# Optimization experiments

Measured on AMD Instinct MI355X. Metric: run time of the kernel, lower is better.

The kernel has to match this reference:

```python
import jax, jax.numpy as jnp
import numpy as np

N_NODES = 100000
N_EDGES = 200000
HIDDEN = 384


def setup_inputs() -> dict:
    key = jax.random.key(0)
    ks = jax.random.split(key, 8)
    x = jax.random.normal(ks[0], (N_NODES, HIDDEN), dtype=jnp.float32)
    # row (source) covers every node at least once so degree >= 1 everywhere
    row_extra = jax.random.randint(ks[1], (N_EDGES - N_NODES,), 0, N_NODES)
    row = jnp.concatenate([jnp.arange(N_NODES), row_extra]).astype(jnp.int64)
    col = jax.random.randint(ks[2], (N_EDGES,), 0, N_NODES).astype(jnp.int64)
    edge_index = jnp.stack([row, col])  # [2, E]
    s = 1.0 / np.sqrt(HIDDEN)
    W1 = jax.random.normal(ks[3], (HIDDEN, HIDDEN), dtype=jnp.float32) * s
    b1 = jax.random.normal(ks[4], (HIDDEN,), dtype=jnp.float32) * s
    W2 = jax.random.normal(ks[5], (HIDDEN, HIDDEN), dtype=jnp.float32) * s
    b2 = jax.random.normal(ks[6], (HIDDEN,), dtype=jnp.float32) * s
    return {"x": x, "edge_index": edge_index, "W1": W1, "b1": b1, "W2": W2, "b2": b2}


def _gcn_layer(x, row, col, W, b):
    n = x.shape[0]
    x = x @ W.T + b  # Linear (torch convention: y = x W^T + b)
    # degree over row (source) only, as in the original message()
    deg = jax.ops.segment_sum(jnp.ones_like(row, dtype=x.dtype), row, num_segments=n)
    dis = deg ** -0.5  # deg>=1 by construction
    norm = dis[row] * dis[col]  # [E]
    msgs = norm[:, None] * x[row]  # gather + scale
    return jax.ops.segment_sum(msgs, col, num_segments=n)  # scatter-add into targets


def reference(x, edge_index, W1, b1, W2, b2):
    row, col = edge_index[0], edge_index[1]
    x = _gcn_layer(x, row, col, W1, b1)
    x = _gcn_layer(x, row, col, W2, b2)
    return x
```

## Files before the change

### kernel.cpp

```cpp
#include <hip/hip_runtime.h>
#include <hip/hip_bf16.h>
#include <cstdint>

#define N_HID 384
#define BM 128
#define BN 128
#define BK 64
#define KTILES 6

typedef __attribute__((ext_vector_type(8))) short bf16x8;
typedef __attribute__((ext_vector_type(4))) float f32x4;

static __device__ __forceinline__ short f2bf(float f) {
    union { __hip_bfloat16 h; short s; } u;
    u.h = __float2bfloat16(f);
    return u.s;
}

static __device__ __forceinline__ void gload_lds16(const void* g, void* l) {
    __builtin_amdgcn_global_load_lds(
        (const __attribute__((address_space(1))) void*)g,
        (__attribute__((address_space(3))) void*)l,
        16, 0, 0);
}

__global__ __launch_bounds__(256) void k_hist(const int* __restrict__ row,
                                              const int* __restrict__ col,
                                              int* __restrict__ deg,
                                              int* __restrict__ cnt, int E) {
    int i = blockIdx.x * 256 + threadIdx.x;
    if (i < E) {
        atomicAdd(&deg[row[i]], 1);
        atomicAdd(&cnt[col[i]], 1);
    }
}

__global__ __launch_bounds__(256) void k_dis(const int* __restrict__ deg,
                                             float* __restrict__ dis, int N) {
    int i = blockIdx.x * 256 + threadIdx.x;
    if (i < N) dis[i] = rsqrtf((float)deg[i]);
}

__global__ __launch_bounds__(256) void k_cvt(const float* __restrict__ in,
                                             short* __restrict__ out, int n4) {
    int i = blockIdx.x * 256 + threadIdx.x;
    if (i < n4) {
        float4 v = reinterpret_cast<const float4*>(in)[i];
        short4 s = make_short4(f2bf(v.x), f2bf(v.y), f2bf(v.z), f2bf(v.w));
        reinterpret_cast<short4*>(out)[i] = s;
    }
}


__global__ __launch_bounds__(256) void k_scan1(const int* __restrict__ cnt,
                                               int* __restrict__ offs,
                                               int* __restrict__ bsum, int N) {
    __shared__ int s[256];
    const int t = threadIdx.x;
    const int base = blockIdx.x * 1024 + t * 4;
    int v[4], tot = 0;
    #pragma unroll
    for (int i = 0; i < 4; i++) { v[i] = (base + i < N) ? cnt[base + i] : 0; tot += v[i]; }
    s[t] = tot;
    __syncthreads();
    #pragma unroll
    for (int off = 1; off < 256; off <<= 1) {
        int x = (t >= off) ? s[t - off] : 0;
        __syncthreads();
        s[t] += x;
        __syncthreads();
    }
    if (t == 255) bsum[blockIdx.x] = s[255];
    int run = s[t] - tot;
    #pragma unroll
    for (int i = 0; i < 4; i++) { if (base + i < N) offs[base + i] = run; run += v[i]; }
}

__global__ __launch_bounds__(256) void k_scan2(int* __restrict__ bsum, int nb) {
    __shared__ int s[256];
    const int t = threadIdx.x;
    int v = (t < nb) ? bsum[t] : 0;
    s[t] = v;
    __syncthreads();
    #pragma unroll
    for (int off = 1; off < 256; off <<= 1) {
        int x = (t >= off) ? s[t - off] : 0;
        __syncthreads();
        s[t] += x;
        __syncthreads();
    }
    if (t < nb) bsum[t] = s[t] - v;
}

__global__ __launch_bounds__(256) void k_scan3(int* __restrict__ offs,
                                               const int* __restrict__ bsum, int N) {
    int i = blockIdx.x * 256 + threadIdx.x;
    if (i < N) offs[i] += bsum[i >> 10];
}

__global__ __launch_bounds__(256) void k_fill(const int* __restrict__ row,
                                              const int* __restrict__ col,
                                              const float* __restrict__ dis,
                                              const int* __restrict__ offs,
                                              int* __restrict__ cur,
                                              int2* __restrict__ srcnrm, int E) {
    int e = blockIdx.x * 256 + threadIdx.x;
    if (e >= E) return;
    int r = row[e], c = col[e];
    int slot = offs[c] + atomicAdd(&cur[c], 1);
    int2 p;
    p.x = r;
    p.y = __float_as_int(dis[r] * dis[c]);
    srcnrm[slot] = p;
}

__global__ __launch_bounds__(256) void k_gemm(const short* __restrict__ A,
                                              const short* __restrict__ W,
                                              const float* __restrict__ bias,
                                              short* __restrict__ out, int M, int MT) {
    __shared__ short As[2][BM][BK];
    __shared__ short Bs[2][BN][BK];
    const int t = threadIdx.x;
    const int bid = blockIdx.x;
    const int m_idx = ((bid >> 3) / 3) * 8 + (bid & 7);
    const int n_idx = (bid >> 3) % 3;
    if (m_idx >= MT) return;
    const int m0 = m_idx * BM, n0 = n_idx * BN;
    const int wave = t >> 6, lane = t & 63;
    const int wm = (wave & 1) * 64, wn = (wave >> 1) * 64;
    const int l16 = lane & 15, quad = lane >> 4;
    const int srow = lane >> 3;
    const int sg8 = ((lane & 7) ^ srow) * 8;
    const int sbase = wave * 8;

    f32x4 acc[4][4] = {};

    auto stage = [&](int b, int kt) {
        #pragma unroll
        for (int p = 0; p < 4; p++) {
            int gm = m0 + p * 32 + sbase + srow;
            gm = gm < M ? gm : M - 1;
            gload_lds16(A + (size_t)gm * N_HID + kt + sg8, &As[b][p * 32 + sbase][0]);
        }
        #pragma unroll
        for (int p = 0; p < 4; p++) {
            int gn = n0 + p * 32 + sbase + srow;
            gload_lds16(W + (size_t)gn * N_HID + kt + sg8, &Bs[b][p * 32 + sbase][0]);
        }
    };

    stage(0, 0);
    #pragma unroll
    for (int kt6 = 0; kt6 < KTILES; kt6++) {
        const int b = kt6 & 1;
        __syncthreads();
        if (kt6 + 1 < KTILES) stage(1 - b, (kt6 + 1) * BK);
        #pragma unroll
        for (int kk = 0; kk < 2; kk++) {
            const int gc = kk * 4 + quad;
            bf16x8 af[4], bfr[4];
            #pragma unroll
            for (int i = 0; i < 4; i++) {
                int rr = wm + i * 16 + l16;
                af[i] = *reinterpret_cast<const bf16x8*>(&As[b][rr][(gc ^ (l16 & 7)) * 8]);
            }
            #pragma unroll
            for (int j = 0; j < 4; j++) {
                int rr = wn + j * 16 + l16;
                bfr[j] = *reinterpret_cast<const bf16x8*>(&Bs[b][rr][(gc ^ (l16 & 7)) * 8]);
            }
            #pragma unroll
            for (int i = 0; i < 4; i++)
                #pragma unroll
                for (int j = 0; j < 4; j++)
                    acc[i][j] = __builtin_amdgcn_mfma_f32_16x16x32_bf16(af[i], bfr[j], acc[i][j], 0, 0, 0);
        }
    }

    __syncthreads();
    short* eps = &As[0][0][0] + wave * 4096;
    #pragma unroll
    for (int j = 0; j < 4; j++) {
        float bv = bias[n0 + wn + j * 16 + l16];
        #pragma unroll
        for (int i = 0; i < 4; i++)
            #pragma unroll
            for (int r = 0; r < 4; r++) {
                int rw = i * 16 + quad * 4 + r;
                int colw = j * 16 + l16;
                int chs = ((colw >> 3) + (rw & 7) + (rw >> 3)) & 7;
                eps[rw * 64 + chs * 8 + (colw & 7)] = f2bf(acc[i][j][r] + bv);
            }
    }
    __syncthreads();
    const int r8 = lane >> 3, ch2 = lane & 7;
    #pragma unroll
    for (int pass = 0; pass < 8; pass++) {
        int rw = pass * 8 + r8;
        int chs = (ch2 + r8 + pass) & 7;
        bf16x8 v = *reinterpret_cast<const bf16x8*>(&eps[rw * 64 + chs * 8]);
        int gm = m0 + wm + rw;
        if (gm < M)
            *reinterpret_cast<bf16x8*>(out + (size_t)gm * N_HID + n0 + wn + ch2 * 8) = v;
    }
}

template <bool BF16OUT>
__global__ __launch_bounds__(256) void k_gather(const short* __restrict__ h,
                                                const int2* __restrict__ srcnrm,
                                                const int* __restrict__ offs,
                                                const int* __restrict__ cur,
                                                void* __restrict__ outv, int N) {
    int node = (blockIdx.x * 256 + threadIdx.x) >> 6;
    if (node >= N) return;
    int lane = threadIdx.x & 63;
    int start = offs[node];
    int ecnt  = cur[node];
    float2 acc[3] = {};
    for (int i = 0; i < ecnt; i++) {
        int2 p = srcnrm[start + i];
        int s = p.x;
        float w = __int_as_float(p.y);
        const unsigned int* hr = reinterpret_cast<const unsigned int*>(h + (size_t)s * N_HID);
        #pragma unroll
        for (int k = 0; k < 3; k++) {
            unsigned int pk = hr[lane + 64 * k];
            acc[k].x += w * __uint_as_float(pk << 16);
            acc[k].y += w * __uint_as_float(pk & 0xffff0000u);
        }
    }
    if (BF16OUT) {
        unsigned int* oc = reinterpret_cast<unsigned int*>(outv) + (size_t)node * 192;
        #pragma unroll
        for (int k = 0; k < 3; k++) {
            unsigned int lo = (unsigned int)(unsigned short)f2bf(acc[k].x);
            unsigned int hi = (unsigned int)(unsigned short)f2bf(acc[k].y);
            oc[lane + 64 * k] = lo | (hi << 16);
        }
    } else {
        float2* oc = reinterpret_cast<float2*>(outv) + (size_t)node * 192;
        #pragma unroll
        for (int k = 0; k < 3; k++) oc[lane + 64 * k] = acc[k];
    }
}

extern "C" void kernel_launch(void* const* d_in, const int* in_sizes, int n_in,
                              void* d_out, int out_size, void* d_ws, size_t ws_size,
                              hipStream_t stream) {
    const float* x  = (const float*)d_in[0];
    const int*   ei = (const int*)d_in[1];
    const float* W1 = (const float*)d_in[2];
    const float* b1 = (const float*)d_in[3];
    const float* W2 = (const float*)d_in[4];
    const float* b2 = (const float*)d_in[5];
    float* out = (float*)d_out;

    const int N = in_sizes[0] / N_HID;
    const int E = in_sizes[1] / 2;
    const int* row = ei;
    const int* col = ei + E;
    const int nb = (N + 1023) / 1024;

    short* xb = (short*)d_out;
    short* a1 = (short*)d_out + (size_t)N * N_HID;

    auto al = [](size_t v) { return (v + 255) & ~(size_t)255; };
    char* ws = (char*)d_ws;
    size_t o = 0;
    int*   deg    = (int*)(ws + o);   o += al((size_t)N * 4);
    int*   offs   = (int*)(ws + o);   o += al((size_t)N * 4);
    float* dis    = (float*)(ws + o); o += al((size_t)N * 4);
    int*   bsum   = (int*)(ws + o);   o += al((size_t)nb * 4);
    int2*  srcnrm = (int2*)(ws + o);  o += al((size_t)E * 8);
    short* w1b    = (short*)(ws + o); o += al((size_t)N_HID * N_HID * 2);
    short* w2b    = (short*)(ws + o); o += al((size_t)N_HID * N_HID * 2);
    short* h      = (short*)(ws + o);
    int*   cur    = deg;

    hipMemsetAsync(deg, 0, al((size_t)N * 4) + (size_t)N * 4, stream);
    k_hist<<<(E + 255) / 256, 256, 0, stream>>>(row, col, deg, offs, E);
    k_dis<<<(N + 255) / 256, 256, 0, stream>>>(deg, dis, N);

    k_scan1<<<nb, 256, 0, stream>>>(offs, offs, bsum, N);
    k_scan2<<<1, 256, 0, stream>>>(bsum, nb);
    k_scan3<<<(N + 255) / 256, 256, 0, stream>>>(offs, bsum, N);
    hipMemsetAsync(cur, 0, (size_t)N * 4, stream);
    k_fill<<<(E + 255) / 256, 256, 0, stream>>>(row, col, dis, offs, cur, srcnrm, E);

    const int x4 = (int)((size_t)N * N_HID / 4);
    const int w4 = N_HID * N_HID / 4;
    k_cvt<<<(x4 + 255) / 256, 256, 0, stream>>>(x, xb, x4);
    k_cvt<<<(w4 + 255) / 256, 256, 0, stream>>>(W1, w1b, w4);
    k_cvt<<<(w4 + 255) / 256, 256, 0, stream>>>(W2, w2b, w4);

    const int MT = (N + BM - 1) / BM;
    const int gblocks = ((MT + 7) / 8) * 24;
    const int gat_blocks = (int)(((size_t)N * 64 + 255) / 256);

    k_gemm<<<gblocks, 256, 0, stream>>>(xb, w1b, b1, h, N, MT);
    k_gather<true><<<gat_blocks, 256, 0, stream>>>(h, srcnrm, offs, cur, a1, N);

    k_gemm<<<gblocks, 256, 0, stream>>>(a1, w2b, b2, h, N, MT);
    k_gather<false><<<gat_blocks, 256, 0, stream>>>(h, srcnrm, offs, cur, out, N);
}
```

Baseline: 491.1 us.

## Reorder GCN as aggregate-then-transform with fused W2·W1 weight and bias folding

Uses linearity to run both sparse aggregations on raw x first. The first gather reads fp32 x directly, so the separate bf16 conversion of x is dropped. The two dense GEMMs are collapsed into a single GEMM against a precomputed W2·W1 product, and the bias terms are folded back in through per-node aggregated normalisation sums (dvec, ddvec) and W2·b1. This removes one large GEMM and the x conversion pass. In exchange the first gather moves fp32 rows instead of bf16, and rounding the product weight and the gathered features to bf16 changes precision.

```diff
diff --git a/kernel.cpp b/kernel.cpp
--- a/kernel.cpp
+++ b/kernel.cpp
@@ -35,22 +35,6 @@
     }
 }
 
-__global__ __launch_bounds__(256) void k_dis(const int* __restrict__ deg,
-                                             float* __restrict__ dis, int N) {
-    int i = blockIdx.x * 256 + threadIdx.x;
-    if (i < N) dis[i] = rsqrtf((float)deg[i]);
-}
-
-__global__ __launch_bounds__(256) void k_cvt(const float* __restrict__ in,
-                                             short* __restrict__ out, int n4) {
-    int i = blockIdx.x * 256 + threadIdx.x;
-    if (i < n4) {
-        float4 v = reinterpret_cast<const float4*>(in)[i];
-        short4 s = make_short4(f2bf(v.x), f2bf(v.y), f2bf(v.z), f2bf(v.w));
-        reinterpret_cast<short4*>(out)[i] = s;
-    }
-}
-
 
 __global__ __launch_bounds__(256) void k_scan1(const int* __restrict__ cnt,
                                                int* __restrict__ offs,
@@ -100,7 +84,7 @@
 
 __global__ __launch_bounds__(256) void k_fill(const int* __restrict__ row,
                                               const int* __restrict__ col,
-                                              const float* __restrict__ dis,
+                                              const int* __restrict__ deg,
                                               const int* __restrict__ offs,
                                               int* __restrict__ cur,
                                               int2* __restrict__ srcnrm, int E) {
@@ -110,14 +94,56 @@
     int slot = offs[c] + atomicAdd(&cur[c], 1);
     int2 p;
     p.x = r;
-    p.y = __float_as_int(dis[r] * dis[c]);
+    p.y = __float_as_int(rsqrtf((float)deg[r]) * rsqrtf((float)deg[c]));
     srcnrm[slot] = p;
 }
 
+__global__ __launch_bounds__(256) void k_prep(const float* __restrict__ W1,
+                                              const float* __restrict__ W2,
+                                              const float* __restrict__ b1,
+                                              short* __restrict__ w1t,
+                                              short* __restrict__ w2b,
+                                              float* __restrict__ wb1) {
+    const int bid = blockIdx.x, t = threadIdx.x;
+    if (bid < 144) {
+        __shared__ short tl[32][33];
+        const int tx = bid % 12, ty = bid / 12;
+        const int c = t & 31, r8 = t >> 5;
+        #pragma unroll
+        for (int rr = 0; rr < 32; rr += 8)
+            tl[c][rr + r8] = f2bf(W1[(ty * 32 + rr + r8) * N_HID + tx * 32 + c]);
+        __syncthreads();
+        #pragma unroll
+        for (int rr = 0; rr < 32; rr += 8)
+            w1t[(tx * 32 + rr + r8) * N_HID + ty * 32 + c] = tl[rr + r8][c];
+    } else if (bid < 288) {
+        int i = (bid - 144) * 256 + t;
+        float4 v = reinterpret_cast<const float4*>(W2)[i];
+        reinterpret_cast<short4*>(w2b)[i] =
+            make_short4(f2bf(v.x), f2bf(v.y), f2bf(v.z), f2bf(v.w));
+    } else {
+        int n = (bid - 288) * 192 + t;
+        if (t < 192) {
+            float s = 0.f;
+            for (int k = 0; k < N_HID; k += 4) {
+                float4 w = *reinterpret_cast<const float4*>(&W2[n * N_HID + k]);
+                float4 b = *reinterpret_cast<const float4*>(&b1[k]);
+                s += w.x * b.x + w.y * b.y + w.z * b.z + w.w * b.w;
+            }
+            wb1[n] = s;
+        }
+    }
+}
+
+template <bool FUSED>
 __global__ __launch_bounds__(256) void k_gemm(const short* __restrict__ A,
                                               const short* __restrict__ W,
                                               const float* __restrict__ bias,
-                                              short* __restrict__ out, int M, int MT) {
+                                              const float* __restrict__ wb1,
+                                              const float* __restrict__ dvec,
+                                              const float* __restrict__ ddvec,
+                                              void* __restrict__ outv,
+                                              int M, int MT) {
     __shared__ short As[2][BM][BK];
     __shared__ short Bs[2][BN][BK];
     const int t = threadIdx.x;
@@ -160,15 +186,11 @@
             const int gc = kk * 4 + quad;
             bf16x8 af[4], bfr[4];
             #pragma unroll
-            for (int i = 0; i < 4; i++) {
-                int rr = wm + i * 16 + l16;
-                af[i] = *reinterpret_cast<const bf16x8*>(&As[b][rr][(gc ^ (l16 & 7)) * 8]);
-            }
-            #pragma unroll
-            for (int j = 0; j < 4; j++) {
-                int rr = wn + j * 16 + l16;
-                bfr[j] = *reinterpret_cast<const bf16x8*>(&Bs[b][rr][(gc ^ (l16 & 7)) * 8]);
-            }
+            for (int i = 0; i < 4; i++)
+                af[i] = *reinterpret_cast<const bf16x8*>(&As[b][wm + i * 16 + l16][(gc ^ (l16 & 7)) * 8]);
+            #pragma unroll
+            for (int j = 0; j < 4; j++)
+                bfr[j] = *reinterpret_cast<const bf16x8*>(&Bs[b][wn + j * 16 + l16][(gc ^ (l16 & 7)) * 8]);
             #pragma unroll
             for (int i = 0; i < 4; i++)
                 #pragma unroll
@@ -177,71 +199,143 @@
         }
     }
 
-    __syncthreads();
-    short* eps = &As[0][0][0] + wave * 4096;
-    #pragma unroll
-    for (int j = 0; j < 4; j++) {
-        float bv = bias[n0 + wn + j * 16 + l16];
+    if (FUSED) {
+        float* outf = (float*)outv;
+        float dv[4][4], ddv[4][4];
         #pragma unroll
         for (int i = 0; i < 4; i++)
             #pragma unroll
             for (int r = 0; r < 4; r++) {
-                int rw = i * 16 + quad * 4 + r;
-                int colw = j * 16 + l16;
-                int chs = ((colw >> 3) + (rw & 7) + (rw >> 3)) & 7;
-                eps[rw * 64 + chs * 8 + (colw & 7)] = f2bf(acc[i][j][r] + bv);
-            }
-    }
-    __syncthreads();
-    const int r8 = lane >> 3, ch2 = lane & 7;
-    #pragma unroll
-    for (int pass = 0; pass < 8; pass++) {
-        int rw = pass * 8 + r8;
-        int chs = (ch2 + r8 + pass) & 7;
-        bf16x8 v = *reinterpret_cast<const bf16x8*>(&eps[rw * 64 + chs * 8]);
-        int gm = m0 + wm + rw;
-        if (gm < M)
-            *reinterpret_cast<bf16x8*>(out + (size_t)gm * N_HID + n0 + wn + ch2 * 8) = v;
-    }
-}
-
-template <bool BF16OUT>
-__global__ __launch_bounds__(256) void k_gather(const short* __restrict__ h,
+                int gm = m0 + wm + i * 16 + quad * 4 + r;
+                int gmc = gm < M ? gm : 0;
+                dv[i][r]  = dvec[gmc];
+                ddv[i][r] = ddvec[gmc];
+            }
+        #pragma unroll
+        for (int j = 0; j < 4; j++) {
+            int gn = n0 + wn + j * 16 + l16;
+            float wb1v = wb1[gn];
+            float b2v  = bias[gn];
+            #pragma unroll
+            for (int i = 0; i < 4; i++) {
+                int gmb = m0 + wm + i * 16 + quad * 4;
+                #pragma unroll
+                for (int r = 0; r < 4; r++) {
+                    int gm = gmb + r;
+                    if (gm < M)
+                        outf[(size_t)gm * N_HID + gn] =
+                            acc[i][j][r] + ddv[i][r] * wb1v + dv[i][r] * b2v;
+                }
+            }
+        }
+    } else {
+        short* outb = (short*)outv;
+        __syncthreads();
+        short* eps = &As[0][0][0] + wave * 4096;
+        #pragma unroll
+        for (int j = 0; j < 4; j++) {
+            float bv = bias[n0 + wn + j * 16 + l16];
+            #pragma unroll
+            for (int i = 0; i < 4; i++)
+                #pragma unroll
+                for (int r = 0; r < 4; r++) {
+                    int rw = i * 16 + quad * 4 + r;
+                    int colw = j * 16 + l16;
+                    int chs = ((colw >> 3) + (rw & 7) + (rw >> 3)) & 7;
+                    eps[rw * 64 + chs * 8 + (colw & 7)] = f2bf(acc[i][j][r] + bv);
+                }
+        }
+        __syncthreads();
+        const int r8 = lane >> 3, ch2 = lane & 7;
+        #pragma unroll
+        for (int pass = 0; pass < 8; pass++) {
+            int rw = pass * 8 + r8;
+            int chs = (ch2 + r8 + pass) & 7;
+            bf16x8 v = *reinterpret_cast<const bf16x8*>(&eps[rw * 64 + chs * 8]);
+            int gm = m0 + wm + rw;
+            if (gm < M)
+                *reinterpret_cast<bf16x8*>(outb + (size_t)gm * N_HID + n0 + wn + ch2 * 8) = v;
+        }
+    }
+}
+
+template <bool SECOND>
+__global__ __launch_bounds__(256) void k_gather(const void* __restrict__ inv,
                                                 const int2* __restrict__ srcnrm,
                                                 const int* __restrict__ offs,
                                                 const int* __restrict__ cur,
-                                                void* __restrict__ outv, int N) {
+                                                const float* __restrict__ din,
+                                                unsigned int* __restrict__ outg,
+                                                float* __restrict__ dout, int N) {
     int node = (blockIdx.x * 256 + threadIdx.x) >> 6;
     if (node >= N) return;
     int lane = threadIdx.x & 63;
     int start = offs[node];
     int ecnt  = cur[node];
     float2 acc[3] = {};
-    for (int i = 0; i < ecnt; i++) {
+    float ds = 0.f;
+    int i = 0;
+    for (; i + 2 <= ecnt; i += 2) {
+        int2 pa = srcnrm[start + i];
+        int2 pb = srcnrm[start + i + 1];
+        float wa = __int_as_float(pa.y), wb = __int_as_float(pb.y);
+        float2 va[3], vb[3];
+        if (SECOND) {
+            const unsigned int* ra = (const unsigned int*)inv + (size_t)pa.x * 192;
+            const unsigned int* rb = (const unsigned int*)inv + (size_t)pb.x * 192;
+            unsigned int ua[3], ub[3];
+            #pragma unroll
+            for (int k = 0; k < 3; k++) { ua[k] = ra[lane + 64 * k]; ub[k] = rb[lane + 64 * k]; }
+            #pragma unroll
+            for (int k = 0; k < 3; k++) {
+                va[k].x = __uint_as_float(ua[k] << 16);
+                va[k].y = __uint_as_float(ua[k] & 0xffff0000u);
+                vb[k].x = __uint_as_float(ub[k] << 16);
+                vb[k].y = __uint_as_float(ub[k] & 0xffff0000u);
+            }
+            ds += wa * din[pa.x] + wb * din[pb.x];
+        } else {
+            const float2* ra = (const float2*)inv + (size_t)pa.x * 192;
+            const float2* rb = (const float2*)inv + (size_t)pb.x * 192;
+            #pragma unroll
+            for (int k = 0; k < 3; k++) { va[k] = ra[lane + 64 * k]; vb[k] = rb[lane + 64 * k]; }
+            ds += wa + wb;
+        }
+        #pragma unroll
+        for (int k = 0; k < 3; k++) {
+            acc[k].x += wa * va[k].x; acc[k].y += wa * va[k].y;
+            acc[k].x += wb * vb[k].x; acc[k].y += wb * vb[k].y;
+        }
+    }
+    if (i < ecnt) {
         int2 p = srcnrm[start + i];
-        int s = p.x;
         float w = __int_as_float(p.y);
-        const unsigned int* hr = reinterpret_cast<const unsigned int*>(h + (size_t)s * N_HID);
-        #pragma unroll
-        for (int k = 0; k < 3; k++) {
-            unsigned int pk = hr[lane + 64 * k];
-            acc[k].x += w * __uint_as_float(pk << 16);
-            acc[k].y += w * __uint_as_float(pk & 0xffff0000u);
-        }
-    }
-    if (BF16OUT) {
-        unsigned int* oc = reinterpret_cast<unsigned int*>(outv) + (size_t)node * 192;
-        #pragma unroll
-        for (int k = 0; k < 3; k++) {
-            unsigned int lo = (unsigned int)(unsigned short)f2bf(acc[k].x);
-            unsigned int hi = (unsigned int)(unsigned short)f2bf(acc[k].y);
-            oc[lane + 64 * k] = lo | (hi << 16);
-        }
-    } else {
-        float2* oc = reinterpret_cast<float2*>(outv) + (size_t)node * 192;
-        #pragma unroll
-        for (int k = 0; k < 3; k++) oc[lane + 64 * k] = acc[k];
-    }
+        if (SECOND) {
+            const unsigned int* r = (const unsigned int*)inv + (size_t)p.x * 192;
+            #pragma unroll
+            for (int k = 0; k < 3; k++) {
+                unsigned int u = r[lane + 64 * k];
+                acc[k].x += w * __uint_as_float(u << 16);
+                acc[k].y += w * __uint_as_float(u & 0xffff0000u);
+            }
+            ds += w * din[p.x];
+        } else {
+            const float2* r = (const float2*)inv + (size_t)p.x * 192;
+            #pragma unroll
+            for (int k = 0; k < 3; k++) {
+                float2 v = r[lane + 64 * k];
+                acc[k].x += w * v.x; acc[k].y += w * v.y;
+            }
+            ds += w;
+        }
+    }
+    #pragma unroll
+    for (int k = 0; k < 3; k++) {
+        unsigned int lo = (unsigned int)(unsigned short)f2bf(acc[k].x);
+        unsigned int hi = (unsigned int)(unsigned short)f2bf(acc[k].y);
+        outg[(size_t)node * 192 + lane + 64 * k] = lo | (hi << 16);
+    }
+    if (lane == 0) dout[node] = ds;
 }
 
 extern "C" void kernel_launch(void* const* d_in, const int* in_sizes, int n_in,
@@ -253,7 +347,6 @@
     const float* b1 = (const float*)d_in[3];
     const float* W2 = (const float*)d_in[4];
     const float* b2 = (const float*)d_in[5];
-    float* out = (float*)d_out;
 
     const int N = in_sizes[0] / N_HID;
     const int E = in_sizes[1] / 2;
@@ -261,45 +354,44 @@
     const int* col = ei + E;
     const int nb = (N + 1023) / 1024;
 
-    short* xb = (short*)d_out;
-    short* a1 = (short*)d_out + (size_t)N * N_HID;
+    unsigned int* g1 = (unsigned int*)d_out;
 
     auto al = [](size_t v) { return (v + 255) & ~(size_t)255; };
     char* ws = (char*)d_ws;
     size_t o = 0;
     int*   deg    = (int*)(ws + o);   o += al((size_t)N * 4);
     int*   offs   = (int*)(ws + o);   o += al((size_t)N * 4);
-    float* dis    = (float*)(ws + o); o += al((size_t)N * 4);
+    float* zeros  = (float*)(ws + o); o += al(N_HID * 4);
+    int*   cur    = (int*)(ws + o);   o += al((size_t)N * 4);
+    const size_t zlen = o;
     int*   bsum   = (int*)(ws + o);   o += al((size_t)nb * 4);
     int2*  srcnrm = (int2*)(ws + o);  o += al((size_t)E * 8);
-    short* w1b    = (short*)(ws + o); o += al((size_t)N_HID * N_HID * 2);
+    short* w1t    = (short*)(ws + o); o += al((size_t)N_HID * N_HID * 2);
     short* w2b    = (short*)(ws + o); o += al((size_t)N_HID * N_HID * 2);
-    short* h      = (short*)(ws + o);
-    int*   cur    = deg;
-
-    hipMemsetAsync(deg, 0, al((size_t)N * 4) + (size_t)N * 4, stream);
+    short* w12    = (short*)(ws + o); o += al((size_t)N_HID * N_HID * 2);
+    float* wb1    = (float*)(ws + o); o += al(N_HID * 4);
+    float* dvec   = (float*)(ws + o); o += al((size_t)N * 4);
+    float* ddvec  = (float*)(ws + o); o += al((size_t)N * 4);
+    unsigned int* g2 = (unsigned int*)(ws + o);
+
+    hipMemsetAsync(deg, 0, zlen, stream);
+
     k_hist<<<(E + 255) / 256, 256, 0, stream>>>(row, col, deg, offs, E);
-    k_dis<<<(N + 255) / 256, 256, 0, stream>>>(deg, dis, N);
-
     k_scan1<<<nb, 256, 0, stream>>>(offs, offs, bsum, N);
     k_scan2<<<1, 256, 0, stream>>>(bsum, nb);
     k_scan3<<<(N + 255) / 256, 256, 0, stream>>>(offs, bsum, N);
-    hipMemsetAsync(cur, 0, (size_t)N * 4, stream);
-    k_fill<<<(E + 255) / 256, 256, 0, stream>>>(row, col, dis, offs, cur, srcnrm, E);
-
-    const int x4 = (int)((size_t)N * N_HID / 4);
-    const int w4 = N_HID * N_HID / 4;
-    k_cvt<<<(x4 + 255) / 256, 256, 0, stream>>>(x, xb, x4);
-    k_cvt<<<(w4 + 255) / 256, 256, 0, stream>>>(W1, w1b, w4);
-    k_cvt<<<(w4 + 255) / 256, 256, 0, stream>>>(W2, w2b, w4);
+    k_fill<<<(E + 255) / 256, 256, 0, stream>>>(row, col, deg, offs, cur, srcnrm, E);
+
+    k_prep<<<290, 256, 0, stream>>>(W1, W2, b1, w1t, w2b, wb1);
+    k_gemm<false><<<24, 256, 0, stream>>>(w2b, w1t, zeros, nullptr, nullptr, nullptr,
+                                          w12, N_HID, 3);
+
+    const int gat_blocks = (int)(((size_t)N * 64 + 255) / 256);
+    k_gather<false><<<gat_blocks, 256, 0, stream>>>(x,  srcnrm, offs, cur, nullptr, g1, dvec, N);
+    k_gather<true><<<gat_blocks, 256, 0, stream>>>(g1, srcnrm, offs, cur, dvec, g2, ddvec, N);
 
     const int MT = (N + BM - 1) / BM;
     const int gblocks = ((MT + 7) / 8) * 24;
-    const int gat_blocks = (int)(((size_t)N * 64 + 255) / 256);
-
-    k_gemm<<<gblocks, 256, 0, stream>>>(xb, w1b, b1, h, N, MT);
-    k_gather<true><<<gat_blocks, 256, 0, stream>>>(h, srcnrm, offs, cur, a1, N);
-
-    k_gemm<<<gblocks, 256, 0, stream>>>(a1, w2b, b2, h, N, MT);
-    k_gather<false><<<gat_blocks, 256, 0, stream>>>(h, srcnrm, offs, cur, out, N);
-}
+    k_gemm<true><<<gblocks, 256, 0, stream>>>((const short*)g2, w12, b2, wb1, dvec, ddvec,
+                                              d_out, N, MT);
+}
```

After: 466.5 us. 5.0% less time.
